# Kernel optimization log

Hardware: AMD Instinct MI355X
Metric: run time of the kernel (lower is better)

## Reference

```python
import jax, jax.numpy as jnp
import numpy as np

SNAPPING_GAIN = 30.0


def setup_inputs() -> dict:
    key = jax.random.key(0)
    k1, k2 = jax.random.split(key)
    latent_coeffs = jax.random.normal(k1, (16, 2048, 1024), dtype=jnp.float32)
    # NMF basis is non-negative; 1024 atoms of dim 900 (30x30 ARC grids)
    basis_vectors = jax.random.uniform(k2, (1024, 900), dtype=jnp.float32)
    return {"latent_coeffs": latent_coeffs, "basis_vectors": basis_vectors}


def reference(latent_coeffs, basis_vectors):
    # [B, K, C] -> sharpened softmax over codes
    probs = jax.nn.softmax(latent_coeffs * SNAPPING_GAIN, axis=-1)
    indices = jnp.argmax(probs, axis=-1)                        # [B, K] int
    one_hot = jax.nn.one_hot(indices, probs.shape[-1], dtype=probs.dtype)
    # straight-through: value == one_hot, gradient flows through probs
    one_hot_st = probs + jax.lax.stop_gradient(one_hot - probs)
    # [B,K,C] @ [C,D] -> [B,K,D] (effectively a row-gather of the basis)
    quantized = jnp.einsum('bkc,cd->bkd', one_hot_st, basis_vectors)
    return quantized, indices
```

## Files before the change

kernel.cpp:

```cpp
#include <hip/hip_runtime.h>


#define C_DIM 1024
#define D_DIM 900

typedef float vfloat4 __attribute__((ext_vector_type(4)));

__global__ __launch_bounds__(256) void basisvq_kernel(
    const float* __restrict__ latent,
    const float* __restrict__ basis,
    float* __restrict__ out_q,
    float* __restrict__ out_idx,
    int rows)
{
    const int lane = threadIdx.x & 63;
    const int wid  = threadIdx.x >> 6;
    const int row  = blockIdx.x * 4 + wid;
    if (row >= rows) return;

    const vfloat4* lrow = reinterpret_cast<const vfloat4*>(latent + (size_t)row * C_DIM);
    vfloat4 v0 = __builtin_nontemporal_load(&lrow[lane]);
    vfloat4 v1 = __builtin_nontemporal_load(&lrow[lane + 64]);
    vfloat4 v2 = __builtin_nontemporal_load(&lrow[lane + 128]);
    vfloat4 v3 = __builtin_nontemporal_load(&lrow[lane + 192]);

    float m = v0[0];
    int   mi = lane * 4;
    #pragma unroll
    for (int e = 1; e < 4; ++e)
        if (v0[e] > m) { m = v0[e]; mi = lane * 4 + e; }
    #pragma unroll
    for (int e = 0; e < 4; ++e) {
        int c = (64 + lane) * 4 + e;
        if (v1[e] > m) { m = v1[e]; mi = c; }
    }
    #pragma unroll
    for (int e = 0; e < 4; ++e) {
        int c = (128 + lane) * 4 + e;
        if (v2[e] > m) { m = v2[e]; mi = c; }
    }
    #pragma unroll
    for (int e = 0; e < 4; ++e) {
        int c = (192 + lane) * 4 + e;
        if (v3[e] > m) { m = v3[e]; mi = c; }
    }

    #pragma unroll
    for (int off = 32; off > 0; off >>= 1) {
        float om = __shfl_xor(m, off, 64);
        int   oi = __shfl_xor(mi, off, 64);
        if (om > m || (om == m && oi < mi)) { m = om; mi = oi; }
    }
    const int idx = mi;

    if (lane == 0) out_idx[row] = (float)idx;

    const vfloat4* b4 = reinterpret_cast<const vfloat4*>(basis + (size_t)idx * D_DIM);
    vfloat4*       o4 = reinterpret_cast<vfloat4*>(out_q + (size_t)row * D_DIM);
    #pragma unroll
    for (int j = 0; j < 4; ++j) {
        int t = 64 * j + lane;
        if (t < 225) {
            vfloat4 bv = b4[t];
            __builtin_nontemporal_store(bv, &o4[t]);
        }
    }
}

extern "C" void kernel_launch(void* const* d_in, const int* in_sizes, int n_in,
                              void* d_out, int out_size, void* d_ws, size_t ws_size,
                              hipStream_t stream) {
    const float* latent = (const float*)d_in[0];
    const float* basis  = (const float*)d_in[1];
    (void)n_in; (void)d_ws; (void)ws_size; (void)out_size;

    const int rows = in_sizes[0] / C_DIM;
    float* out_q   = (float*)d_out;
    float* out_idx = (float*)d_out + (size_t)rows * D_DIM;

    const int blocks = (rows + 3) / 4;
    basisvq_kernel<<<blocks, 256, 0, stream>>>(latent, basis, out_q, out_idx, rows);
}
```

Before: 50.51 us.

## Split fused argmax+gather kernel into separate argmax and gather kernels

Splits the single kernel into an argmax kernel that reads the latent rows and writes indices, and a gather kernel that reads those indices back and copies the basis rows into the output. The aim is to decouple the read-heavy phase from the write-heavy phase so each kernel streams one direction of traffic without a dependent gather stalling each wave. In exchange it adds a second launch and an extra round trip of the index array through memory.

```diff
diff --git a/kernel.cpp b/kernel.cpp
--- a/kernel.cpp
+++ b/kernel.cpp
@@ -6,10 +6,8 @@
 
 typedef float vfloat4 __attribute__((ext_vector_type(4)));
 
-__global__ __launch_bounds__(256) void basisvq_kernel(
+__global__ __launch_bounds__(256) void argmax_kernel(
     const float* __restrict__ latent,
-    const float* __restrict__ basis,
-    float* __restrict__ out_q,
     float* __restrict__ out_idx,
     int rows)
 {
@@ -30,20 +28,14 @@
     for (int e = 1; e < 4; ++e)
         if (v0[e] > m) { m = v0[e]; mi = lane * 4 + e; }
     #pragma unroll
-    for (int e = 0; e < 4; ++e) {
-        int c = (64 + lane) * 4 + e;
-        if (v1[e] > m) { m = v1[e]; mi = c; }
-    }
+    for (int e = 0; e < 4; ++e)
+        if (v1[e] > m) { m = v1[e]; mi = (64 + lane) * 4 + e; }
     #pragma unroll
-    for (int e = 0; e < 4; ++e) {
-        int c = (128 + lane) * 4 + e;
-        if (v2[e] > m) { m = v2[e]; mi = c; }
-    }
+    for (int e = 0; e < 4; ++e)
+        if (v2[e] > m) { m = v2[e]; mi = (128 + lane) * 4 + e; }
     #pragma unroll
-    for (int e = 0; e < 4; ++e) {
-        int c = (192 + lane) * 4 + e;
-        if (v3[e] > m) { m = v3[e]; mi = c; }
-    }
+    for (int e = 0; e < 4; ++e)
+        if (v3[e] > m) { m = v3[e]; mi = (192 + lane) * 4 + e; }
 
     #pragma unroll
     for (int off = 32; off > 0; off >>= 1) {
@@ -51,9 +43,22 @@
         int   oi = __shfl_xor(mi, off, 64);
         if (om > m || (om == m && oi < mi)) { m = om; mi = oi; }
     }
-    const int idx = mi;
 
-    if (lane == 0) out_idx[row] = (float)idx;
+    if (lane == 0) __builtin_nontemporal_store((float)mi, &out_idx[row]);
+}
+
+__global__ __launch_bounds__(256) void gather_kernel(
+    const float* __restrict__ basis,
+    const float* __restrict__ out_idx,
+    float* __restrict__ out_q,
+    int rows)
+{
+    const int lane = threadIdx.x & 63;
+    const int wid  = threadIdx.x >> 6;
+    const int row  = blockIdx.x * 4 + wid;
+    if (row >= rows) return;
+
+    const int idx = (int)out_idx[row];
 
     const vfloat4* b4 = reinterpret_cast<const vfloat4*>(basis + (size_t)idx * D_DIM);
     vfloat4*       o4 = reinterpret_cast<vfloat4*>(out_q + (size_t)row * D_DIM);
@@ -79,5 +84,6 @@
     float* out_idx = (float*)d_out + (size_t)rows * D_DIM;
 
     const int blocks = (rows + 3) / 4;
-    basisvq_kernel<<<blocks, 256, 0, stream>>>(latent, basis, out_q, out_idx, rows);
+    argmax_kernel<<<blocks, 256, 0, stream>>>(latent, out_idx, rows);
+    gather_kernel<<<blocks, 256, 0, stream>>>(basis, out_idx, out_q, rows);
 }
```

Result: slower. 51.79 us (+2.5%).
